# Performance work log

Measured on AMD Instinct MI355X. Metric: run time of the kernel, lower is better.

## Reference

```python
import jax, jax.numpy as jnp
import numpy as np

B, T, EMB = 2, 2048, 2048
NH, NKV, HD, VHD = 16, 4, 128, 128
N_REP = NH // NKV
ROPE_DIM, ROPE_THETA = 64, 10000.0
WIN = 1024
MLPD = 8192
CS = 2048  # cache size == T: single prefill fills the cache
K_MASK = jnp.finfo(jnp.bfloat16).min
SCALING = HD ** -0.5


def _rope_sincos(positions, rope_dim, theta):
    fraction = jnp.arange(0, rope_dim, 2, dtype=jnp.float32) / rope_dim
    inv_freq = 1.0 / (theta ** fraction)
    ang = jnp.einsum('BT,k->BTk', positions.astype(jnp.float32), inv_freq,
                     precision=jax.lax.Precision.HIGHEST)
    sin, cos = jnp.sin(ang), jnp.cos(ang)
    return jnp.concatenate([sin, sin], -1), jnp.concatenate([cos, cos], -1)


def _rotate_half(x):
    h = x.shape[-1] // 2
    return jnp.concatenate([-x[..., h:], x[..., :h]], -1)


def _apply_rope_partial(x, sin, cos, rope_dim):
    x_rope, x_nope = x[..., :rope_dim], x[..., rope_dim:]
    s, c = sin[:, :, None, :], cos[:, :, None, :]
    x_rope = x_rope * c + _rotate_half(x_rope) * s
    return jnp.concatenate([x_rope, x_nope], -1).astype(x.dtype)


def _rms_norm(x, scale, eps=1e-6):
    xf = x.astype(jnp.float32)
    var = jnp.mean(jnp.square(xf), axis=-1, keepdims=True)
    return (xf * jax.lax.rsqrt(var + eps) * (1.0 + scale)).astype(x.dtype)


def _repeat_kv(h, n_rep):
    if n_rep == 1:
        return h
    b, s, k, d = h.shape
    return jnp.repeat(h[:, :, :, None, :], n_rep, axis=3).reshape(b, s, k * n_rep, d)


def setup_inputs() -> dict:
    key = jax.random.key(0)
    ks = jax.random.split(key, 12)
    s = 0.02
    return {
        'x': jax.random.normal(ks[0], (B, T, EMB), jnp.float32),
        'segment_ids': jnp.ones((B, T), jnp.int32),
        'wq': jax.random.normal(ks[1], (EMB, NH, HD), jnp.float32) * s,
        'wk': jax.random.normal(ks[2], (EMB, NKV, HD), jnp.float32) * s,
        'wv': jax.random.normal(ks[3], (EMB, NKV, VHD), jnp.float32) * s,
        'wo': jax.random.normal(ks[4], (NH, VHD, EMB), jnp.float32) * s,
        'sink_bias': jax.random.normal(ks[5], (NH,), jnp.float32) * s,
        'gate_w': jax.random.normal(ks[6], (EMB, MLPD), jnp.float32) * s,
        'up_w': jax.random.normal(ks[7], (EMB, MLPD), jnp.float32) * s,
        'down_w': jax.random.normal(ks[8], (MLPD, EMB), jnp.float32) * s,
        'norm1_scale': jax.random.normal(ks[9], (EMB,), jnp.float32) * s,
        'norm2_scale': jax.random.normal(ks[10], (EMB,), jnp.float32) * s,
        'k_cache': jnp.zeros((B, CS, NKV, HD), jnp.float32),
        'v_cache': jnp.zeros((B, CS, NKV, VHD), jnp.float32),
    }


def reference(x, segment_ids, wq, wk, wv, wo, sink_bias, gate_w, up_w, down_w,
              norm1_scale, norm2_scale, k_cache, v_cache):
    b, t, _ = x.shape
    cs = k_cache.shape[1]
    cur_ind = jnp.zeros((), jnp.int32)  # fresh cache (prefill)

    # --- attention branch (pre-norm) ---
    h = _rms_norm(x, norm1_scale)
    q = jnp.einsum('BTD,DNH->BTNH', h, wq)
    k = jnp.einsum('BSD,DKH->BSKH', h, wk)
    v = jnp.einsum('BSD,DKV->BSKV', h, wv)

    left_pads = jnp.sum(jnp.cumsum(segment_ids != 0, axis=-1) == 0, -1).astype(jnp.int32)
    start_ind = left_pads  # start_ind initialized to -1 -> set to left_pads
    ar = jnp.arange(t, dtype=jnp.int32)
    first = jnp.argmax(segment_ids, axis=1).astype(jnp.int32)
    positions = jnp.where(segment_ids != 0, ar[None, :] - first[:, None], 2 ** 30) + cur_ind

    sin, cos = _rope_sincos(positions, ROPE_DIM, ROPE_THETA)
    q = _apply_rope_partial(q, sin, cos, ROPE_DIM)
    k = _apply_rope_partial(k, sin, cos, ROPE_DIM)

    k_cache = jax.lax.dynamic_update_slice(k_cache, k, (0, cur_ind, 0, 0))
    v_cache = jax.lax.dynamic_update_slice(v_cache, v, (0, cur_ind, 0, 0))

    kc = _repeat_kv(k_cache, N_REP)  # [B,S,N,H]
    vc = _repeat_kv(v_cache, N_REP)  # [B,S,N,V]

    attn_logits = jnp.einsum('BTNH,BSNH->BTNS', q, kc) * SCALING

    q_pos = cur_ind + ar[None, :] - start_ind[:, None]                      # [B,T]
    ts = jnp.arange(cs, dtype=jnp.int32)
    kv_segment_ids = (ts[None, :] >= start_ind[:, None]) & (ts[None, :] < cur_ind + t)
    k_pos = ts[None, :] - start_ind[:, None]                                # [B,S]
    causal_mask = k_pos[:, None, :] <= q_pos[:, :, None]
    segment_mask = kv_segment_ids[:, None, :] == segment_ids[:, :, None]
    window_mask = k_pos[:, None, :] >= q_pos[:, :, None] - (WIN - 1)
    final_mask = causal_mask & segment_mask & window_mask                    # [B,T,S]

    attn_logits = jnp.where(final_mask[:, :, None, :], attn_logits, K_MASK)

    # learned sink bias: extra logit column, dropped after softmax
    sink = jnp.broadcast_to(sink_bias[None, None, :, None], (b, t, NH, 1))
    attn_logits = jnp.concatenate([attn_logits, sink], axis=-1)
    attn_weights = jax.nn.softmax(attn_logits.astype(jnp.float32), axis=-1).astype(attn_logits.dtype)
    attn_weights = attn_weights[..., :-1]

    attn_out = jnp.einsum('BTNS,BSNV->BTNV', attn_weights, vc)
    attn_out = jnp.einsum('BTNV,NVD->BTD', attn_out, wo)

    x = x + attn_out

    # --- MLP branch (pre-norm, SwiGLU) ---
    h = _rms_norm(x, norm2_scale)
    mlp_out = (jax.nn.silu(h @ gate_w) * (h @ up_w)) @ down_w
    return x + mlp_out
```

## Files before the change

kernel.cpp:

```cpp
#include <hip/hip_runtime.h>
#include <hip/hip_bf16.h>
#include <stdint.h>

#define B_    2
#define T_    2048
#define EMB_  2048
#define NH_   16
#define NKV_  4
#define HD_   128
#define MLPD_ 8192
#define WIN_  1024
#define BT_   (B_ * T_)
#define QKVN_ 3072

typedef __bf16 bf16;
typedef __bf16 bf16x8 __attribute__((ext_vector_type(8)));
typedef float  f32x4  __attribute__((ext_vector_type(4)));

__device__ __forceinline__ bf16 f2b(float f) {
  __hip_bfloat16 h = __float2bfloat16(f);
  return *reinterpret_cast<bf16*>(&h);
}
__device__ __forceinline__ float b2f(bf16 b) {
  __hip_bfloat16 h = *reinterpret_cast<__hip_bfloat16*>(&b);
  return __bfloat162float(h);
}

__device__ __forceinline__ void load_lds16(const void* g, void* l) {
  __builtin_amdgcn_global_load_lds(
      (const __attribute__((address_space(1))) void*)g,
      (__attribute__((address_space(3))) void*)l, 16, 0, 0);
}

__global__ __launch_bounds__(256) void transpose_kernel(
    const float* __restrict__ in, bf16* __restrict__ out, int R, int C)
{
  __shared__ float tile[32][33];
  const int tx = threadIdx.x, ty = threadIdx.y;
  const int c0 = blockIdx.x * 32, r0 = blockIdx.y * 32;
  #pragma unroll
  for (int i = 0; i < 32; i += 8)
    tile[ty + i][tx] = in[(long)(r0 + ty + i) * C + c0 + tx];
  __syncthreads();
  #pragma unroll
  for (int i = 0; i < 32; i += 8)
    out[(long)(c0 + ty + i) * R + r0 + tx] = f2b(tile[tx][ty + i]);
}

__global__ __launch_bounds__(256) void rmsnorm_kernel(
    const float* __restrict__ x, const float* __restrict__ scale,
    bf16* __restrict__ out)
{
  const long row = blockIdx.x;
  const float* xr = x + row * EMB_;
  bf16* orow = out + row * EMB_;
  const float4 v0 = ((const float4*)xr)[threadIdx.x];
  const float4 v1 = ((const float4*)xr)[threadIdx.x + 256];
  float ss = v0.x*v0.x + v0.y*v0.y + v0.z*v0.z + v0.w*v0.w
           + v1.x*v1.x + v1.y*v1.y + v1.z*v1.z + v1.w*v1.w;
  #pragma unroll
  for (int off = 32; off >= 1; off >>= 1) ss += __shfl_xor(ss, off, 64);
  __shared__ float red[4];
  if ((threadIdx.x & 63) == 0) red[threadIdx.x >> 6] = ss;
  __syncthreads();
  const float tot = red[0] + red[1] + red[2] + red[3];
  const float rs = rsqrtf(tot * (1.0f / EMB_) + 1e-6f);
  const float4 s0 = ((const float4*)scale)[threadIdx.x];
  const float4 s1 = ((const float4*)scale)[threadIdx.x + 256];
  const int c0 = threadIdx.x * 4;
  orow[c0 + 0]    = f2b(v0.x * rs * (1.0f + s0.x));
  orow[c0 + 1]    = f2b(v0.y * rs * (1.0f + s0.y));
  orow[c0 + 2]    = f2b(v0.z * rs * (1.0f + s0.z));
  orow[c0 + 3]    = f2b(v0.w * rs * (1.0f + s0.w));
  orow[c0 + 1024] = f2b(v1.x * rs * (1.0f + s1.x));
  orow[c0 + 1025] = f2b(v1.y * rs * (1.0f + s1.y));
  orow[c0 + 1026] = f2b(v1.z * rs * (1.0f + s1.z));
  orow[c0 + 1027] = f2b(v1.w * rs * (1.0f + s1.w));
}

template <int EPI>
__global__ __launch_bounds__(256) void gemm_kernel(
    const bf16* __restrict__ A, const bf16* __restrict__ Bt,
    void* __restrict__ out, const float* __restrict__ res,
    int M, int N, int K)
{
  __shared__ __align__(16) bf16 As[128 * 32];
  __shared__ __align__(16) bf16 Bs[128 * 32];
  const int tid  = threadIdx.x;
  const int wave = tid >> 6, lane = tid & 63;
  const int bm = blockIdx.y << 7, bn = blockIdx.x << 7;
  const int wm = (wave & 1) << 6, wn = (wave >> 1) << 6;
  const int l16 = lane & 15, quad = lane >> 4;
  const int srow = lane >> 2, scol = (lane & 3) << 3;

  const bf16* Ap = A  + (long)(bm + wave * 32 + srow) * K + scol;
  const bf16* Bp = Bt + (long)(bn + wave * 32 + srow) * K + scol;
  char* ldsA = (char*)As + wave * 2048;
  char* ldsB = (char*)Bs + wave * 2048;

  f32x4 acc[4][4] = {};

  for (int k0 = 0; k0 < K; k0 += 32) {
    __syncthreads();
    #pragma unroll
    for (int j = 0; j < 2; ++j) {
      load_lds16(Ap + (long)j * 16 * K + k0, ldsA + j * 1024);
      load_lds16(Bp + (long)j * 16 * K + k0, ldsB + j * 1024);
    }
    __syncthreads();
    bf16x8 af[4], bfr[4];
    #pragma unroll
    for (int i = 0; i < 4; ++i) {
      af[i]  = *(const bf16x8*)&As[(wm + i * 16 + l16) * 32 + quad * 8];
      bfr[i] = *(const bf16x8*)&Bs[(wn + i * 16 + l16) * 32 + quad * 8];
    }
    #pragma unroll
    for (int mb = 0; mb < 4; ++mb)
      #pragma unroll
      for (int nb = 0; nb < 4; ++nb)
        acc[mb][nb] = __builtin_amdgcn_mfma_f32_16x16x32_bf16(af[mb], bfr[nb], acc[mb][nb], 0, 0, 0);
  }

  const int crow = bm + wm + (quad << 2);
  const int ccol = bn + wn + l16;
  #pragma unroll
  for (int mb = 0; mb < 4; ++mb)
    #pragma unroll
    for (int nb = 0; nb < 4; ++nb)
      #pragma unroll
      for (int r = 0; r < 4; ++r) {
        const long idx = (long)(crow + mb * 16 + r) * N + (ccol + nb * 16);
        const float v = acc[mb][nb][r];
        if (EPI == 0) {
          ((bf16*)out)[idx] = f2b(v);
        } else {
          ((float*)out)[idx] = v + res[idx];
        }
      }
}

__global__ __launch_bounds__(512) void mlp_gateup_kernel(
    const bf16* __restrict__ A, const bf16* __restrict__ Bg,
    const bf16* __restrict__ Bu, bf16* __restrict__ out,
    int M, int N, int K)
{
  __shared__ __align__(16) char smem[49152];
  const int tid = threadIdx.x;
  const int wave = tid >> 6, lane = tid & 63;
  const int role = wave >> 2, wq = wave & 3;
  const int wm = (wq & 1) << 6, wn = (wq >> 1) << 6;
  const int l16 = lane & 15, quad = lane >> 4;
  const int srow = lane >> 2, scol = (lane & 3) << 3;

  const int bm = blockIdx.y << 7, bn = blockIdx.x << 7;

  const bf16* sp[6]; char* dp[6];
  #pragma unroll
  for (int j = 0; j < 6; ++j) {
    const int c = 6 * wave + j;
    const int buf = c >> 4, idx = c & 15, kh = idx >> 3, r8 = idx & 7;
    const bf16* gbase = (buf == 0) ? A + (long)bm * K
                      : (buf == 1) ? Bg + (long)bn * K
                                   : Bu + (long)bn * K;
    sp[j] = gbase + (long)(r8 * 16 + srow) * K + kh * 32 + scol;
    dp[j] = smem + buf * 16384 + kh * 8192 + r8 * 1024;
  }
  const bf16* Asb = (const bf16*)smem;
  const bf16* Bsb = (const bf16*)(smem + 16384 + role * 16384);

  f32x4 acc[4][4] = {};

  for (int k0 = 0; k0 < K; k0 += 64) {
    __syncthreads();
    #pragma unroll
    for (int j = 0; j < 6; ++j) load_lds16(sp[j] + k0, dp[j]);
    __syncthreads();
    #pragma unroll
    for (int kh = 0; kh < 2; ++kh) {
      bf16x8 af[4], bfr[4];
      #pragma unroll
      for (int i = 0; i < 4; ++i) {
        af[i]  = *(const bf16x8*)&Asb[kh * 4096 + (wm + i * 16 + l16) * 32 + quad * 8];
        bfr[i] = *(const bf16x8*)&Bsb[kh * 4096 + (wn + i * 16 + l16) * 32 + quad * 8];
      }
      #pragma unroll
      for (int mb = 0; mb < 4; ++mb)
        #pragma unroll
        for (int nb = 0; nb < 4; ++nb)
          acc[mb][nb] = __builtin_amdgcn_mfma_f32_16x16x32_bf16(af[mb], bfr[nb], acc[mb][nb], 0, 0, 0);
    }
  }

  __syncthreads();
  bf16* Ex = (bf16*)smem;
  const int rw = wm + (quad << 2), cw = wn + l16;
  if (role == 0) {
    #pragma unroll
    for (int mb = 0; mb < 4; ++mb)
      #pragma unroll
      for (int nb = 0; nb < 4; ++nb)
        #pragma unroll
        for (int r = 0; r < 4; ++r) {
          const float g = acc[mb][nb][r];
          Ex[(rw + mb * 16 + r) * 128 + cw + nb * 16] = f2b(g / (1.0f + __expf(-g)));
        }
  }
  __syncthreads();
  if (role == 1) {
    #pragma unroll
    for (int mb = 0; mb < 4; ++mb)
      #pragma unroll
      for (int nb = 0; nb < 4; ++nb)
        #pragma unroll
        for (int r = 0; r < 4; ++r) {
          const float sg = b2f(Ex[(rw + mb * 16 + r) * 128 + cw + nb * 16]);
          out[(long)(bm + rw + mb * 16 + r) * N + bn + cw + nb * 16] =
              f2b(acc[mb][nb][r] * sg);
        }
  }
}

__global__ __launch_bounds__(512) void down_kernel(
    const bf16* __restrict__ A, const bf16* __restrict__ Bt,
    float* __restrict__ out, const float* __restrict__ res,
    int M, int N, int K)
{
  __shared__ __align__(16) char smem[24576];
  const int tid = threadIdx.x;
  const int wave = tid >> 6, lane = tid & 63;
  const int role = wave >> 2, wq = wave & 3;
  const int wm = (wq & 1) << 6, wn = (wq >> 1) << 6;
  const int l16 = lane & 15, quad = lane >> 4;
  const int srow = lane >> 2, scol = (lane & 3) << 3;

  const int bm = blockIdx.y << 8, bn = blockIdx.x << 7;

  const bf16* sp[3]; char* dp[3];
  #pragma unroll
  for (int j = 0; j < 3; ++j) {
    const int c = 3 * wave + j;
    const int buf = c >> 3, r0 = (c & 7) << 4;
    const bf16* gbase = (buf == 0) ? A + (long)bm * K
                      : (buf == 1) ? A + (long)(bm + 128) * K
                                   : Bt + (long)bn * K;
    sp[j] = gbase + (long)(r0 + srow) * K + scol;
    dp[j] = smem + buf * 8192 + (c & 7) * 1024;
  }
  const bf16* Asb = (const bf16*)(smem + role * 8192);
  const bf16* Bsb = (const bf16*)(smem + 16384);

  f32x4 acc[4][4] = {};

  for (int k0 = 0; k0 < K; k0 += 32) {
    __syncthreads();
    #pragma unroll
    for (int j = 0; j < 3; ++j) load_lds16(sp[j] + k0, dp[j]);
    __syncthreads();
    bf16x8 af[4], bfr[4];
    #pragma unroll
    for (int i = 0; i < 4; ++i) {
      af[i]  = *(const bf16x8*)&Asb[(wm + i * 16 + l16) * 32 + quad * 8];
      bfr[i] = *(const bf16x8*)&Bsb[(wn + i * 16 + l16) * 32 + quad * 8];
    }
    #pragma unroll
    for (int mb = 0; mb < 4; ++mb)
      #pragma unroll
      for (int nb = 0; nb < 4; ++nb)
        acc[mb][nb] = __builtin_amdgcn_mfma_f32_16x16x32_bf16(af[mb], bfr[nb], acc[mb][nb], 0, 0, 0);
  }

  const int crow = bm + role * 128 + wm + (quad << 2);
  const int ccol = bn + wn + l16;
  #pragma unroll
  for (int mb = 0; mb < 4; ++mb)
    #pragma unroll
    for (int nb = 0; nb < 4; ++nb)
      #pragma unroll
      for (int r = 0; r < 4; ++r) {
        const long idx = (long)(crow + mb * 16 + r) * N + (ccol + nb * 16);
        out[idx] = acc[mb][nb][r] + res[idx];
      }
}

__global__ __launch_bounds__(256) void rope_kernel(
    const bf16* __restrict__ qkv, bf16* __restrict__ Q,
    bf16* __restrict__ K, bf16* __restrict__ VT)
{
  const int t = blockIdx.x, b = blockIdx.y;
  const bf16* row = qkv + (long)(b * T_ + t) * QKVN_;
  const float tf = (float)t;
  for (int idx = threadIdx.x; idx < NH_ * HD_; idx += 256) {
    const int head = idx >> 7, hd = idx & 127;
    const float v = b2f(row[idx]);
    float o;
    if (hd < 64) {
      const int j = hd & 31;
      const float ang = tf * expf(-(float)j * 0.28782313662425574f);
      const float sn = sinf(ang), cs = cosf(ang);
      o = (hd < 32) ? (v * cs - b2f(row[idx + 32]) * sn)
                    : (v * cs + b2f(row[idx - 32]) * sn);
    } else o = v;
    Q[((long)(b * NH_ + head) * T_ + t) * HD_ + hd] = f2b(o);
  }
  for (int idx = threadIdx.x; idx < NKV_ * HD_; idx += 256) {
    const int kv = idx >> 7, hd = idx & 127;
    const float v = b2f(row[NH_ * HD_ + idx]);
    float o;
    if (hd < 64) {
      const int j = hd & 31;
      const float ang = tf * expf(-(float)j * 0.28782313662425574f);
      const float sn = sinf(ang), cs = cosf(ang);
      o = (hd < 32) ? (v * cs - b2f(row[NH_ * HD_ + idx + 32]) * sn)
                    : (v * cs + b2f(row[NH_ * HD_ + idx - 32]) * sn);
    } else o = v;
    K[((long)(b * NKV_ + kv) * T_ + t) * HD_ + hd] = f2b(o);
  }
  for (int idx = threadIdx.x; idx < NKV_ * HD_; idx += 256) {
    const int kv = idx >> 7, vd = idx & 127;
    VT[((long)(b * NKV_ + kv) * HD_ + vd) * T_ + t] = row[(NH_ + NKV_) * HD_ + idx];
  }
}

__global__ __launch_bounds__(256) void attn_kernel(
    const bf16* __restrict__ Q, const bf16* __restrict__ Kg,
    const bf16* __restrict__ VTg, const float* __restrict__ sink,
    bf16* __restrict__ attnb)
{
  __shared__ __align__(16) bf16 Qs[64 * 136];
  __shared__ __align__(16) bf16 Ks[64 * 136];
  __shared__ __align__(16) bf16 Vs[128 * 72];
  __shared__ __align__(16) bf16 Ps[64 * 72];

  const int qt = blockIdx.x;
  const int bh = blockIdx.y;
  const int b = bh >> 4, h = bh & 15;
  const int kvh = h >> 2;
  const int t0 = qt * 64;
  const int tid = threadIdx.x;
  const int wave = tid >> 6, lane = tid & 63;
  const int quad = lane >> 4, l16 = lane & 15;

  const bf16* Qp = Q + ((long)(b * NH_ + h) * T_ + t0) * HD_;
  #pragma unroll
  for (int c = tid; c < 1024; c += 256) {
    const int r = c >> 4, cc = (c & 15) << 3;
    *(uint4*)&Qs[r * 136 + cc] = *(const uint4*)&Qp[r * HD_ + cc];
  }

  float m_i[4], l_i[4];
  const float sb = sink[h];
  #pragma unroll
  for (int r = 0; r < 4; ++r) { m_i[r] = sb; l_i[r] = 1.0f; }
  f32x4 Oacc[8] = {};

  const int st_lo = (qt > 16) ? (qt - 16) : 0;
  for (int st = st_lo; st <= qt; ++st) {
    const int s0 = st * 64;
    __syncthreads();
    const bf16* Kp = Kg + ((long)(b * NKV_ + kvh) * T_ + s0) * HD_;
    #pragma unroll
    for (int c = tid; c < 1024; c += 256) {
      const int r = c >> 4, cc = (c & 15) << 3;
      *(uint4*)&Ks[r * 136 + cc] = *(const uint4*)&Kp[r * HD_ + cc];
    }
    const bf16* Vp = VTg + (long)(b * NKV_ + kvh) * HD_ * T_ + s0;
    #pragma unroll
    for (int c = tid; c < 1024; c += 256) {
      const int r = c >> 3, cc = (c & 7) << 3;
      *(uint4*)&Vs[r * 72 + cc] = *(const uint4*)&Vp[(long)r * T_ + cc];
    }
    __syncthreads();

    f32x4 sacc[4] = {};
    #pragma unroll
    for (int kb = 0; kb < 4; ++kb) {
      const bf16x8 aq = *(const bf16x8*)&Qs[(wave * 16 + l16) * 136 + kb * 32 + quad * 8];
      #pragma unroll
      for (int nb = 0; nb < 4; ++nb) {
        const bf16x8 bk = *(const bf16x8*)&Ks[(nb * 16 + l16) * 136 + kb * 32 + quad * 8];
        sacc[nb] = __builtin_amdgcn_mfma_f32_16x16x32_bf16(aq, bk, sacc[nb], 0, 0, 0);
      }
    }

    float sv[4][4];
    float rmax[4] = {-INFINITY, -INFINITY, -INFINITY, -INFINITY};
    const int colb = s0 + l16;
    const int rowb = t0 + wave * 16 + quad * 4;
    #pragma unroll
    for (int nb = 0; nb < 4; ++nb)
      #pragma unroll
      for (int r = 0; r < 4; ++r) {
        float v = sacc[nb][r] * 0.08838834764831845f;
        const int s = colb + nb * 16, tq = rowb + r;
        if (s > tq || s < tq - (WIN_ - 1)) v = -INFINITY;
        sv[nb][r] = v;
        rmax[r] = fmaxf(rmax[r], v);
      }
    #pragma unroll
    for (int r = 0; r < 4; ++r)
      #pragma unroll
      for (int off = 1; off < 16; off <<= 1)
        rmax[r] = fmaxf(rmax[r], __shfl_xor(rmax[r], off, 64));
    float alpha[4], rsum[4];
    #pragma unroll
    for (int r = 0; r < 4; ++r) {
      const float mn = fmaxf(m_i[r], rmax[r]);
      alpha[r] = __expf(m_i[r] - mn);
      m_i[r] = mn;
      rsum[r] = 0.0f;
    }
    #pragma unroll
    for (int nb = 0; nb < 4; ++nb)
      #pragma unroll
      for (int r = 0; r < 4; ++r) {
        const float p = __expf(sv[nb][r] - m_i[r]);
        rsum[r] += p;
        Ps[(wave * 16 + quad * 4 + r) * 72 + nb * 16 + l16] = f2b(p);
      }
    #pragma unroll
    for (int r = 0; r < 4; ++r) {
      #pragma unroll
      for (int off = 1; off < 16; off <<= 1)
        rsum[r] += __shfl_xor(rsum[r], off, 64);
      l_i[r] = l_i[r] * alpha[r] + rsum[r];
    }
    #pragma unroll
    for (int nb = 0; nb < 8; ++nb)
      #pragma unroll
      for (int r = 0; r < 4; ++r)
        Oacc[nb][r] *= alpha[r];
    __syncthreads();

    #pragma unroll
    for (int ks = 0; ks < 2; ++ks) {
      const bf16x8 ap = *(const bf16x8*)&Ps[(wave * 16 + l16) * 72 + ks * 32 + quad * 8];
      #pragma unroll
      for (int nb = 0; nb < 8; ++nb) {
        const bf16x8 bv = *(const bf16x8*)&Vs[(nb * 16 + l16) * 72 + ks * 32 + quad * 8];
        Oacc[nb] = __builtin_amdgcn_mfma_f32_16x16x32_bf16(ap, bv, Oacc[nb], 0, 0, 0);
      }
    }
  }

  float rcp[4];
  #pragma unroll
  for (int r = 0; r < 4; ++r) rcp[r] = 1.0f / l_i[r];
  bf16* outp = attnb + ((long)(b * T_ + t0 + wave * 16 + quad * 4)) * EMB_ + h * HD_ + l16;
  #pragma unroll
  for (int nb = 0; nb < 8; ++nb)
    #pragma unroll
    for (int r = 0; r < 4; ++r)
      outp[(long)r * EMB_ + nb * 16] = f2b(Oacc[nb][r] * rcp[r]);
}

extern "C" void kernel_launch(void* const* d_in, const int* in_sizes, int n_in,
                              void* d_out, int out_size, void* d_ws, size_t ws_size,
                              hipStream_t stream)
{
  (void)in_sizes; (void)n_in; (void)out_size; (void)ws_size;
  const float* x    = (const float*)d_in[0];
  const float* wq   = (const float*)d_in[2];
  const float* wk   = (const float*)d_in[3];
  const float* wv   = (const float*)d_in[4];
  const float* wo   = (const float*)d_in[5];
  const float* sink = (const float*)d_in[6];
  const float* gw   = (const float*)d_in[7];
  const float* uw   = (const float*)d_in[8];
  const float* dw   = (const float*)d_in[9];
  const float* n1   = (const float*)d_in[10];
  const float* n2   = (const float*)d_in[11];

  char* base = (char*)d_ws;
  bf16*  hbuf  = (bf16*)base;
  char*  R1    = base + (size_t)16777216;
  char*  R2    = R1   + (size_t)67108864;
  bf16*  mact  = (bf16*)(R2 + (size_t)33554432);

  bf16* qkv   = (bf16*)R1;
  bf16* Qb    = (bf16*)(R1 + 25165824);
  bf16* Kb    = (bf16*)(R1 + 41943040);
  bf16* VTb   = (bf16*)(R1 + 46137344);
  bf16* attnb = (bf16*)R1;
  bf16* wqkvT = (bf16*)R2;
  bf16* woT   = (bf16*)(R2 + 12582912);
  bf16* gateT = (bf16*)R1;
  bf16* upT   = (bf16*)(R1 + 33554432);
  bf16* downT = (bf16*)R2;
  float* x1   = (float*)d_out;

  const dim3 tb(32, 8);
  transpose_kernel<<<dim3( 64,  64), tb, 0, stream>>>(wq, wqkvT,                      EMB_, EMB_);
  transpose_kernel<<<dim3( 16,  64), tb, 0, stream>>>(wk, wqkvT + (size_t)2048*EMB_,  EMB_, 512);
  transpose_kernel<<<dim3( 16,  64), tb, 0, stream>>>(wv, wqkvT + (size_t)2560*EMB_,  EMB_, 512);
  transpose_kernel<<<dim3( 64,  64), tb, 0, stream>>>(wo, woT,                        EMB_, EMB_);

  rmsnorm_kernel<<<BT_, 256, 0, stream>>>(x, n1, hbuf);
  gemm_kernel<0><<<dim3(QKVN_/128, BT_/128), 256, 0, stream>>>(hbuf, wqkvT, qkv, nullptr, BT_, QKVN_, EMB_);
  rope_kernel<<<dim3(T_, B_), 256, 0, stream>>>(qkv, Qb, Kb, VTb);
  attn_kernel<<<dim3(T_/64, B_*NH_), 256, 0, stream>>>(Qb, Kb, VTb, sink, attnb);
  gemm_kernel<1><<<dim3(EMB_/128, BT_/128), 256, 0, stream>>>(attnb, woT, x1, x, BT_, EMB_, EMB_);

  rmsnorm_kernel<<<BT_, 256, 0, stream>>>(x1, n2, hbuf);
  transpose_kernel<<<dim3(256,  64), tb, 0, stream>>>(gw, gateT, EMB_, MLPD_);
  transpose_kernel<<<dim3(256,  64), tb, 0, stream>>>(uw, upT,   EMB_, MLPD_);
  mlp_gateup_kernel<<<dim3(MLPD_/128, BT_/128), 512, 0, stream>>>(hbuf, gateT, upT, mact, BT_, MLPD_, EMB_);
  transpose_kernel<<<dim3( 64, 256), tb, 0, stream>>>(dw, downT, MLPD_, EMB_);
  down_kernel<<<dim3(EMB_/128, BT_/256), 512, 0, stream>>>(mact, downT, (float*)d_out, x1, BT_, EMB_, MLPD_);
}
```

Baseline: 1.122 ms.

## Rewrite MLP gate/up GEMM with 256x256 tiles, interleaved weights, double-buffered LDS

The gate and up weight transposes now write into one buffer, interleaved in 16-row groups, so a single GEMM can compute both projections and pair them in registers for the SiLU-multiply epilogue. The new gate/up kernel uses 256x256 block tiles and 128KB of double-buffered LDS filled by direct global-to-LDS loads. It also uses an XOR-swizzled LDS layout, explicit barrier and waitcnt scheduling, and setprio around MFMA clusters. The aim is more operand reuse per LDS load, global loads overlapped with compute, and no LDS round trip in the epilogue. The cost is heavy LDS use that limits occupancy, plus hand-placed synchronisation that is fragile.

Result: faster. 1.097 ms (-2.2%).

```diff
diff --git a/kernel.cpp b/kernel.cpp
--- a/kernel.cpp
+++ b/kernel.cpp
@@ -33,7 +33,8 @@
 }
 
 __global__ __launch_bounds__(256) void transpose_kernel(
-    const float* __restrict__ in, bf16* __restrict__ out, int R, int C)
+    const float* __restrict__ in, bf16* __restrict__ out, int R, int C,
+    int rmul, int radd)
 {
   __shared__ float tile[32][33];
   const int tx = threadIdx.x, ty = threadIdx.y;
@@ -43,8 +44,11 @@
     tile[ty + i][tx] = in[(long)(r0 + ty + i) * C + c0 + tx];
   __syncthreads();
   #pragma unroll
-  for (int i = 0; i < 32; i += 8)
-    out[(long)(c0 + ty + i) * R + r0 + tx] = f2b(tile[tx][ty + i]);
+  for (int i = 0; i < 32; i += 8) {
+    const int oc = c0 + ty + i;
+    const int orow = (oc & 15) + (((oc >> 4) * rmul + radd) << 4);
+    out[(long)orow * R + r0 + tx] = f2b(tile[tx][ty + i]);
+  }
 }
 
 __global__ __launch_bounds__(256) void rmsnorm_kernel(
@@ -139,85 +143,139 @@
       }
 }
 
-__global__ __launch_bounds__(512) void mlp_gateup_kernel(
-    const bf16* __restrict__ A, const bf16* __restrict__ Bg,
-    const bf16* __restrict__ Bu, bf16* __restrict__ out,
-    int M, int N, int K)
-{
-  __shared__ __align__(16) char smem[49152];
-  const int tid = threadIdx.x;
+#define GU_BAR()  do { asm volatile("" ::: "memory"); \
+                       __builtin_amdgcn_s_barrier(); \
+                       asm volatile("" ::: "memory"); } while (0)
+#define GU_LGK0() do { asm volatile("s_waitcnt lgkmcnt(0)" ::: "memory"); \
+                       __builtin_amdgcn_sched_barrier(0); } while (0)
+#define GU_VMC0() asm volatile("s_waitcnt vmcnt(0)" ::: "memory")
+
+#define GU_STAGE(TILE, BB) do { \
+    _Pragma("unroll") \
+    for (int j_ = 0; j_ < 8; ++j_) \
+      load_lds16(srcp[j_] + (long)(TILE) * 64, smem + (BB) + dstoff[j_]); \
+  } while (0)
+
+#define GU_READA(BB, MH) do { \
+    const char* ab_ = smem + (BB) + wroff; \
+    _Pragma("unroll") \
+    for (int mb_ = 0; mb_ < 4; ++mb_) { \
+      const int rb_ = ((MH) * 64 + mb_ * 16 + l16) * 128; \
+      afr[mb_][0] = *(const bf16x8*)(ab_ + rb_ + koff0); \
+      afr[mb_][1] = *(const bf16x8*)(ab_ + rb_ + koff1); \
+    } } while (0)
+
+#define GU_READB(BB, NH) do { \
+    const char* bb_ = smem + (BB) + 32768 + bhoff; \
+    _Pragma("unroll") \
+    for (int nb_ = 0; nb_ < 2; ++nb_) { \
+      const int rb_ = (brow0 + (NH) * 32 + nb_ * 16) * 128; \
+      bfr[NH][nb_][0] = *(const bf16x8*)(bb_ + rb_ + koff0); \
+      bfr[NH][nb_][1] = *(const bf16x8*)(bb_ + rb_ + koff1); \
+    } } while (0)
+
+#define GU_MFMAQ(MH, NH) do { \
+    _Pragma("unroll") \
+    for (int mb_ = 0; mb_ < 4; ++mb_) \
+      _Pragma("unroll") \
+      for (int nb_ = 0; nb_ < 2; ++nb_) { \
+        f32x4* a_ = &acc[(MH) * 4 + mb_][(NH) * 2 + nb_]; \
+        *a_ = __builtin_amdgcn_mfma_f32_16x16x32_bf16(afr[mb_][0], bfr[NH][nb_][0], *a_, 0, 0, 0); \
+        *a_ = __builtin_amdgcn_mfma_f32_16x16x32_bf16(afr[mb_][1], bfr[NH][nb_][1], *a_, 0, 0, 0); \
+      } } while (0)
+
+__global__ __launch_bounds__(512, 2) void mlp_gateup256_kernel(
+    const bf16* __restrict__ A, const bf16* __restrict__ Bc,
+    bf16* __restrict__ out, int M, int Ncat, int K)
+{
+  (void)M;
+  __shared__ __align__(16) char smem[131072];
+  const int tid  = threadIdx.x;
   const int wave = tid >> 6, lane = tid & 63;
-  const int role = wave >> 2, wq = wave & 3;
-  const int wm = (wq & 1) << 6, wn = (wq >> 1) << 6;
-  const int l16 = lane & 15, quad = lane >> 4;
-  const int srow = lane >> 2, scol = (lane & 3) << 3;
-
-  const int bm = blockIdx.y << 7, bn = blockIdx.x << 7;
-
-  const bf16* sp[6]; char* dp[6];
-  #pragma unroll
-  for (int j = 0; j < 6; ++j) {
-    const int c = 6 * wave + j;
-    const int buf = c >> 4, idx = c & 15, kh = idx >> 3, r8 = idx & 7;
-    const bf16* gbase = (buf == 0) ? A + (long)bm * K
-                      : (buf == 1) ? Bg + (long)bn * K
-                                   : Bu + (long)bn * K;
-    sp[j] = gbase + (long)(r8 * 16 + srow) * K + kh * 32 + scol;
-    dp[j] = smem + buf * 16384 + kh * 8192 + r8 * 1024;
-  }
-  const bf16* Asb = (const bf16*)smem;
-  const bf16* Bsb = (const bf16*)(smem + 16384 + role * 16384);
-
-  f32x4 acc[4][4] = {};
-
-  for (int k0 = 0; k0 < K; k0 += 64) {
-    __syncthreads();
-    #pragma unroll
-    for (int j = 0; j < 6; ++j) load_lds16(sp[j] + k0, dp[j]);
-    __syncthreads();
-    #pragma unroll
-    for (int kh = 0; kh < 2; ++kh) {
-      bf16x8 af[4], bfr[4];
-      #pragma unroll
-      for (int i = 0; i < 4; ++i) {
-        af[i]  = *(const bf16x8*)&Asb[kh * 4096 + (wm + i * 16 + l16) * 32 + quad * 8];
-        bfr[i] = *(const bf16x8*)&Bsb[kh * 4096 + (wn + i * 16 + l16) * 32 + quad * 8];
-      }
-      #pragma unroll
-      for (int mb = 0; mb < 4; ++mb)
-        #pragma unroll
-        for (int nb = 0; nb < 4; ++nb)
-          acc[mb][nb] = __builtin_amdgcn_mfma_f32_16x16x32_bf16(af[mb], bfr[nb], acc[mb][nb], 0, 0, 0);
-    }
-  }
-
-  __syncthreads();
-  bf16* Ex = (bf16*)smem;
-  const int rw = wm + (quad << 2), cw = wn + l16;
-  if (role == 0) {
-    #pragma unroll
-    for (int mb = 0; mb < 4; ++mb)
-      #pragma unroll
-      for (int nb = 0; nb < 4; ++nb)
-        #pragma unroll
-        for (int r = 0; r < 4; ++r) {
-          const float g = acc[mb][nb][r];
-          Ex[(rw + mb * 16 + r) * 128 + cw + nb * 16] = f2b(g / (1.0f + __expf(-g)));
-        }
-  }
-  __syncthreads();
-  if (role == 1) {
-    #pragma unroll
-    for (int mb = 0; mb < 4; ++mb)
-      #pragma unroll
-      for (int nb = 0; nb < 4; ++nb)
-        #pragma unroll
-        for (int r = 0; r < 4; ++r) {
-          const float sg = b2f(Ex[(rw + mb * 16 + r) * 128 + cw + nb * 16]);
-          out[(long)(bm + rw + mb * 16 + r) * N + bn + cw + nb * 16] =
-              f2b(acc[mb][nb][r] * sg);
-        }
-  }
+  const int quad = lane >> 4, l16 = lane & 15;
+  const int wr = wave >> 2, wc = wave & 3;
+  const int bm = blockIdx.y << 8, bn = blockIdx.x << 8;
+  const int KT = K >> 6;
+
+  const int koff0 = (quad * 16) ^ ((l16 & 7) << 4);
+  const int koff1 = koff0 ^ 64;
+  const int wroff = wr * 16384;
+  const int bhoff = (wc >> 1) * 16384;
+  const int brow0 = (wc & 1) * 64 + l16;
+
+  const int srow = lane >> 3;
+  const int scol = ((lane & 7) ^ srow) << 3;
+  const bf16* srcp[8]; int dstoff[8];
+  #pragma unroll
+  for (int op = 0; op < 2; ++op)
+    #pragma unroll
+    for (int h = 0; h < 2; ++h)
+      #pragma unroll
+      for (int g = 0; g < 2; ++g) {
+        const int j = op * 4 + h * 2 + g;
+        const int grow = (op ? bn : bm) + h * 128 + g * 64 + wave * 8 + srow;
+        srcp[j] = (op ? Bc : A) + (long)grow * K + scol;
+        dstoff[j] = op * 32768 + h * 16384 + g * 8192 + wave * 1024;
+      }
+
+  f32x4 acc[8][4] = {};
+  bf16x8 afr[4][2];
+  bf16x8 bfr[2][2][2];
+
+  GU_STAGE(0, 0);
+  GU_VMC0();
+  GU_BAR();
+
+  #pragma unroll 1
+  for (int t = 0; t < KT; t += 2) {
+    GU_STAGE(t + 1, 65536);
+    GU_READA(0, 0); GU_READB(0, 0);
+    GU_BAR(); GU_LGK0();
+    __builtin_amdgcn_s_setprio(1); GU_MFMAQ(0, 0); __builtin_amdgcn_s_setprio(0);
+    GU_BAR();
+    GU_READB(0, 1);
+    GU_BAR(); GU_LGK0();
+    __builtin_amdgcn_s_setprio(1); GU_MFMAQ(0, 1); __builtin_amdgcn_s_setprio(0);
+    GU_BAR();
+    GU_READA(0, 1);
+    GU_BAR(); GU_LGK0();
+    __builtin_amdgcn_s_setprio(1); GU_MFMAQ(1, 1); __builtin_amdgcn_s_setprio(0);
+    GU_BAR();
+    __builtin_amdgcn_s_setprio(1); GU_MFMAQ(1, 0); __builtin_amdgcn_s_setprio(0);
+    GU_VMC0();
+    GU_BAR();
+    if (t + 2 < KT) GU_STAGE(t + 2, 0);
+    GU_READA(65536, 0); GU_READB(65536, 0);
+    GU_BAR(); GU_LGK0();
+    __builtin_amdgcn_s_setprio(1); GU_MFMAQ(0, 0); __builtin_amdgcn_s_setprio(0);
+    GU_BAR();
+    GU_READB(65536, 1);
+    GU_BAR(); GU_LGK0();
+    __builtin_amdgcn_s_setprio(1); GU_MFMAQ(0, 1); __builtin_amdgcn_s_setprio(0);
+    GU_BAR();
+    GU_READA(65536, 1);
+    GU_BAR(); GU_LGK0();
+    __builtin_amdgcn_s_setprio(1); GU_MFMAQ(1, 1); __builtin_amdgcn_s_setprio(0);
+    GU_BAR();
+    __builtin_amdgcn_s_setprio(1); GU_MFMAQ(1, 0); __builtin_amdgcn_s_setprio(0);
+    GU_VMC0();
+    GU_BAR();
+  }
+
+  const long NO = Ncat >> 1;
+  const int orow0 = bm + wr * 128 + (quad << 2);
+  const int ocol  = (bn >> 1) + wc * 32 + l16;
+  #pragma unroll
+  for (int ma = 0; ma < 8; ++ma)
+    #pragma unroll
+    for (int nh = 0; nh < 2; ++nh)
+      #pragma unroll
+      for (int r = 0; r < 4; ++r) {
+        const float g = acc[ma][nh * 2][r];
+        const float u = acc[ma][nh * 2 + 1][r];
+        out[(long)(orow0 + ma * 16 + r) * NO + ocol + nh * 16] =
+            f2b(g / (1.0f + __expf(-g)) * u);
+      }
 }
 
 __global__ __launch_bounds__(512) void down_kernel(
@@ -483,16 +541,15 @@
   bf16* attnb = (bf16*)R1;
   bf16* wqkvT = (bf16*)R2;
   bf16* woT   = (bf16*)(R2 + 12582912);
-  bf16* gateT = (bf16*)R1;
-  bf16* upT   = (bf16*)(R1 + 33554432);
+  bf16* Bcat  = (bf16*)R1;
   bf16* downT = (bf16*)R2;
   float* x1   = (float*)d_out;
 
   const dim3 tb(32, 8);
-  transpose_kernel<<<dim3( 64,  64), tb, 0, stream>>>(wq, wqkvT,                      EMB_, EMB_);
-  transpose_kernel<<<dim3( 16,  64), tb, 0, stream>>>(wk, wqkvT + (size_t)2048*EMB_,  EMB_, 512);
-  transpose_kernel<<<dim3( 16,  64), tb, 0, stream>>>(wv, wqkvT + (size_t)2560*EMB_,  EMB_, 512);
-  transpose_kernel<<<dim3( 64,  64), tb, 0, stream>>>(wo, woT,                        EMB_, EMB_);
+  transpose_kernel<<<dim3( 64,  64), tb, 0, stream>>>(wq, wqkvT,                      EMB_, EMB_, 1, 0);
+  transpose_kernel<<<dim3( 16,  64), tb, 0, stream>>>(wk, wqkvT + (size_t)2048*EMB_,  EMB_, 512, 1, 0);
+  transpose_kernel<<<dim3( 16,  64), tb, 0, stream>>>(wv, wqkvT + (size_t)2560*EMB_,  EMB_, 512, 1, 0);
+  transpose_kernel<<<dim3( 64,  64), tb, 0, stream>>>(wo, woT,                        EMB_, EMB_, 1, 0);
 
   rmsnorm_kernel<<<BT_, 256, 0, stream>>>(x, n1, hbuf);
   gemm_kernel<0><<<dim3(QKVN_/128, BT_/128), 256, 0, stream>>>(hbuf, wqkvT, qkv, nullptr, BT_, QKVN_, EMB_);
@@ -501,9 +558,9 @@
   gemm_kernel<1><<<dim3(EMB_/128, BT_/128), 256, 0, stream>>>(attnb, woT, x1, x, BT_, EMB_, EMB_);
 
   rmsnorm_kernel<<<BT_, 256, 0, stream>>>(x1, n2, hbuf);
-  transpose_kernel<<<dim3(256,  64), tb, 0, stream>>>(gw, gateT, EMB_, MLPD_);
-  transpose_kernel<<<dim3(256,  64), tb, 0, stream>>>(uw, upT,   EMB_, MLPD_);
-  mlp_gateup_kernel<<<dim3(MLPD_/128, BT_/128), 512, 0, stream>>>(hbuf, gateT, upT, mact, BT_, MLPD_, EMB_);
-  transpose_kernel<<<dim3( 64, 256), tb, 0, stream>>>(dw, downT, MLPD_, EMB_);
+  transpose_kernel<<<dim3(256,  64), tb, 0, stream>>>(gw, Bcat, EMB_, MLPD_, 2, 0);
+  transpose_kernel<<<dim3(256,  64), tb, 0, stream>>>(uw, Bcat, EMB_, MLPD_, 2, 1);
+  mlp_gateup256_kernel<<<dim3((2*MLPD_)/256, BT_/256), 512, 0, stream>>>(hbuf, Bcat, mact, BT_, 2*MLPD_, EMB_);
+  transpose_kernel<<<dim3( 64, 256), tb, 0, stream>>>(dw, downT, MLPD_, EMB_, 1, 0);
   down_kernel<<<dim3(EMB_/128, BT_/256), 512, 0, stream>>>(mact, downT, (float*)d_out, x1, BT_, EMB_, MLPD_);
 }
```
